# Optimization experiments

Measured on AMD Instinct MI355X. Metric: run time of the kernel, lower is better.

Reference implementation:

```python
import jax, jax.numpy as jnp
import numpy as np

EPS = 1e-5
LAMBDA_REG = 1.0
ALPHA_ENTROPY = 0.5
ALPHA_DIVERSITY = 0.5

B, N, D, K = 32, 1024, 256, 512  # batch, tokens, dim_embed, num_embed


def setup_inputs() -> dict:
    key = jax.random.key(0)
    k0, k1, k2 = jax.random.split(key, 3)
    inputs = jax.random.normal(k0, (B, N, D), dtype=jnp.float32)
    gamma = jnp.ones((D,), jnp.float32)
    beta = jnp.zeros((D,), jnp.float32)
    # keras 'uniform' initializer default: U(-0.05, 0.05)
    embed_w = jax.random.uniform(k1, (D, K), jnp.float32, -0.05, 0.05)
    # keras 'random_normal' default: stddev=0.05
    d_w = jax.random.normal(k2, (D, D), jnp.float32) * 0.05
    d_b = jnp.zeros((D,), jnp.float32)
    return {"inputs": inputs, "gamma": gamma, "beta": beta,
            "embed_w": embed_w, "d_w": d_w, "d_b": d_b}


def _project_columns_to_simplex(P_sol):
    # P_sol: (K, M); project each column onto the probability simplex.
    P_t = P_sol.T                                   # (M, K)
    sorted_P = -jnp.sort(-P_t, axis=1)              # descending
    cumsum = jnp.cumsum(sorted_P, axis=1)
    k = jnp.arange(1, K + 1, dtype=P_t.dtype)
    thresholds = (cumsum - 1.0) / k
    valid = (sorted_P > thresholds).astype(jnp.int32)
    max_idx = jnp.argmax(valid * jnp.arange(K, dtype=jnp.int32), axis=1)  # (M,)
    sel_cumsum = jnp.take_along_axis(cumsum, max_idx[:, None], axis=1)[:, 0]
    theta = (sel_cumsum - 1.0) / (max_idx.astype(P_t.dtype) + 1.0)
    return jax.nn.relu(P_t - theta[:, None]).T      # (K, M)


def _forward(inputs, gamma, beta, embed_w, d_w, d_b):
    # dense + layernorm
    x = jnp.matmul(inputs, d_w) + d_b
    mean = jnp.mean(x, axis=-1, keepdims=True)
    var = jnp.var(x, axis=-1, keepdims=True)
    x = gamma * ((x - mean) / jnp.sqrt(var + EPS)) + beta

    flat = x.reshape(-1, D)                          # (M, D)
    flat_sg = jax.lax.stop_gradient(flat)

    # hard assignment (VQ-style, on detached encodings)
    dists = (jnp.sum(flat_sg ** 2, axis=1, keepdims=True)
             + jnp.sum(embed_w ** 2, axis=0, keepdims=True)
             - 2.0 * jnp.matmul(flat_sg, embed_w))   # (M, K)
    assign = jnp.argmin(dists, axis=1)
    P_tilde = jax.nn.one_hot(assign, K, dtype=jnp.float32).T  # (K, M)

    # regularized least squares: (C^T C + lam I) P = C^T Z + lam P_tilde
    C = embed_w                                       # (D, K)
    Z = flat.T                                        # (D, M)
    A = jnp.matmul(C.T, C) + LAMBDA_REG * jnp.eye(K, dtype=jnp.float32)
    b = jnp.matmul(C.T, Z) + LAMBDA_REG * P_tilde     # (K, M)
    P_sol = jnp.linalg.solve(A, b)
    P_proj = _project_columns_to_simplex(P_sol)       # (K, M)

    out_P_proj = P_proj.T.reshape(B, N, K)

    # perplexity
    p_j = jnp.mean(out_P_proj, axis=(0, 1))
    p_j = jnp.clip(p_j, 1e-10, 1.0 - 1e-9)
    p_j = p_j / jnp.sum(p_j)
    entropy_bits = -jnp.sum(p_j * jnp.log(p_j) / jnp.log(2.0))
    perplexity = jnp.power(2.0, entropy_bits)

    Zq_flat = jnp.matmul(C, P_proj).T                 # (M, D)

    # entropy regularizer
    p_mean = jnp.mean(out_P_proj, axis=(0, 1))
    p_mn = p_mean / (jnp.sum(p_mean) + EPS)
    entropy_reg = -jnp.sum(p_mn * jnp.log(p_mn + EPS))

    # diversity loss on l2-normalized codebook columns
    norm_cb = embed_w / jnp.sqrt(jnp.maximum(jnp.sum(embed_w ** 2, axis=0, keepdims=True), 1e-12))
    sims = jnp.matmul(norm_cb.T, norm_cb)
    masked = sims * (1.0 - jnp.eye(K, dtype=jnp.float32))
    diversity_loss = jnp.mean(jax.nn.relu(masked))

    primary_loss = jnp.mean((Zq_flat - flat) ** 2)  # discrete_loss=False path
    loss = primary_loss + ALPHA_ENTROPY * entropy_reg + ALPHA_DIVERSITY * diversity_loss

    Zq = Zq_flat.reshape(B, N, D)
    return Zq, out_P_proj, loss, perplexity


def reference(inputs, gamma, beta, embed_w, d_w, d_b):
    return _forward(inputs, gamma, beta, embed_w, d_w, d_b)
```

## Files before the change

kernel.cpp:

```cpp
#include <hip/hip_runtime.h>
#include <math.h>


#define M_ 32768
#define D_ 256
#define K_ 512
#define TAU 0.006f

typedef short bf16x8 __attribute__((ext_vector_type(8)));
typedef unsigned short u16x8 __attribute__((ext_vector_type(8)));
typedef unsigned short u16x4 __attribute__((ext_vector_type(4)));
typedef float f32x4 __attribute__((ext_vector_type(4)));

#define LSTR 56

__device__ inline void split_rne(float f, unsigned short& h, unsigned short& l)
{
    unsigned int u = __float_as_uint(f);
    unsigned int uh = u + (0x7FFFu + ((u >> 16) & 1u));
    h = (unsigned short)(uh >> 16);
    float fh = __uint_as_float(((unsigned int)h) << 16);
    float r = f - fh;
    l = (unsigned short)(__float_as_uint(r) >> 16);
}

__device__ inline unsigned short rne16(float f)
{
    unsigned int u = __float_as_uint(f);
    u += 0x7FFFu + ((u >> 16) & 1u);
    return (unsigned short)(u >> 16);
}

template<int EPI>
__global__ __launch_bounds__(256)
void mfma_gemm(const unsigned short* __restrict__ Ah,
               const unsigned short* __restrict__ Bh,
               float* __restrict__ Out, int Kd, int N,
               const float* __restrict__ AinvM, const int* __restrict__ assign,
               const float* Zref, float* __restrict__ lossPart)
{
    __shared__ unsigned short sA[128*LSTR];
    __shared__ unsigned short sB[128*LSTR];
    __shared__ float red[256];
    const int tid = threadIdx.x;
    const int m0 = blockIdx.y * 128, n0 = blockIdx.x * 128;
    const int w = tid >> 6, lane = tid & 63;
    const int wr = (w & 1) * 64, wc = (w >> 1) * 64;
    const int cg = lane >> 4, cr = lane & 15;

    f32x4 acc[4][4];
    const f32x4 z4 = {0.f, 0.f, 0.f, 0.f};
#pragma unroll
    for (int i = 0; i < 4; ++i)
#pragma unroll
        for (int j = 0; j < 4; ++j) acc[i][j] = z4;

    const int sr = tid >> 1;
    const int sk = (tid & 1) * 16;
    const int soff = sr * LSTR + sk;
    const unsigned short* Agh = Ah + (size_t)(m0 + sr) * Kd + sk;
    const unsigned short* Bgh = Bh + (size_t)(n0 + sr) * Kd + sk;

    for (int kb = 0; kb < Kd; kb += 32) {
        *(u16x8*)&sA[soff]     = *(const u16x8*)(Agh + kb);
        *(u16x8*)&sA[soff + 8] = *(const u16x8*)(Agh + kb + 8);
        *(u16x8*)&sB[soff]     = *(const u16x8*)(Bgh + kb);
        *(u16x8*)&sB[soff + 8] = *(const u16x8*)(Bgh + kb + 8);
        __syncthreads();
        bf16x8 ah[4], bh[4];
#pragma unroll
        for (int f = 0; f < 4; ++f) {
            ah[f] = *(const bf16x8*)&sA[(wr + f*16 + cr) * LSTR + cg*8];
            bh[f] = *(const bf16x8*)&sB[(wc + f*16 + cr) * LSTR + cg*8];
        }
#pragma unroll
        for (int i = 0; i < 4; ++i)
#pragma unroll
            for (int j = 0; j < 4; ++j)
                acc[i][j] = __builtin_amdgcn_mfma_f32_16x16x32_bf16(ah[i], bh[j], acc[i][j], 0, 0, 0);
        __syncthreads();
    }

    if (EPI == 2) {
#pragma unroll
        for (int i = 0; i < 4; ++i) {
#pragma unroll
            for (int q = 0; q < 4; ++q) {
                const int row = m0 + wr + i*16 + cg*4 + q;
                const int am = assign[row];
                const float* Arow = AinvM + (size_t)am * K_ + n0 + wc;
#pragma unroll
                for (int j = 0; j < 4; ++j)
                    Out[(size_t)row * N + n0 + wc + j*16 + cr] =
                        acc[i][j][q] + Arow[j*16 + cr];
            }
        }
    } else {
        float lsum = 0.f;
#pragma unroll
        for (int i = 0; i < 4; ++i) {
#pragma unroll
            for (int q = 0; q < 4; ++q) {
                const int row = m0 + wr + i*16 + cg*4 + q;
#pragma unroll
                for (int j = 0; j < 4; ++j) {
                    const int col = n0 + wc + j*16 + cr;
                    const float v = acc[i][j][q];
                    const float zv = Zref[(size_t)row * N + col];
                    const float d = v - zv;
                    lsum += d * d;
                    Out[(size_t)row * N + col] = v;
                }
            }
        }
        red[tid] = lsum;
        __syncthreads();
        for (int s = 128; s > 0; s >>= 1) {
            if (tid < s) red[tid] += red[tid + s];
            __syncthreads();
        }
        if (tid == 0) lossPart[blockIdx.y * gridDim.x + blockIdx.x] = red[0];
    }
}

__global__ __launch_bounds__(256)
void score_mfma_argmin(const unsigned short* __restrict__ Zh, const unsigned short* __restrict__ Zl,
                       const unsigned short* __restrict__ Bth, const unsigned short* __restrict__ Btl,
                       const float* __restrict__ cn2, const float* __restrict__ zn2,
                       float* __restrict__ PV, float* __restrict__ PB,
                       int* __restrict__ PI)
{
    __shared__ unsigned short sAh[128*LSTR], sAl[128*LSTR];
    __shared__ unsigned short sBh[128*LSTR], sBl[128*LSTR];
    __shared__ float l1v[128][2], l2v[128][2];
    __shared__ int   liv[128][2];
    const int tid = threadIdx.x;
    const int m0 = blockIdx.y * 128, n0 = blockIdx.x * 128;
    const int w = tid >> 6, lane = tid & 63;
    const int wr = (w & 1) * 64, wc = (w >> 1) * 64;
    const int cg = lane >> 4, cr = lane & 15;

    f32x4 acc[4][4];
    const f32x4 z4 = {0.f, 0.f, 0.f, 0.f};
#pragma unroll
    for (int i = 0; i < 4; ++i)
#pragma unroll
        for (int j = 0; j < 4; ++j) acc[i][j] = z4;

    const int sr = tid >> 1;
    const int sk = (tid & 1) * 16;
    const int soff = sr * LSTR + sk;
    const unsigned short* Ah = Zh  + (size_t)(m0 + sr) * D_ + sk;
    const unsigned short* Al = Zl  + (size_t)(m0 + sr) * D_ + sk;
    const unsigned short* Bh = Bth + (size_t)(n0 + sr) * D_ + sk;
    const unsigned short* Bl = Btl + (size_t)(n0 + sr) * D_ + sk;

    for (int kb = 0; kb < D_; kb += 32) {
        *(u16x8*)&sAh[soff]     = *(const u16x8*)(Ah + kb);
        *(u16x8*)&sAh[soff + 8] = *(const u16x8*)(Ah + kb + 8);
        *(u16x8*)&sAl[soff]     = *(const u16x8*)(Al + kb);
        *(u16x8*)&sAl[soff + 8] = *(const u16x8*)(Al + kb + 8);
        *(u16x8*)&sBh[soff]     = *(const u16x8*)(Bh + kb);
        *(u16x8*)&sBh[soff + 8] = *(const u16x8*)(Bh + kb + 8);
        *(u16x8*)&sBl[soff]     = *(const u16x8*)(Bl + kb);
        *(u16x8*)&sBl[soff + 8] = *(const u16x8*)(Bl + kb + 8);
        __syncthreads();
        bf16x8 ah[4], al[4], bh[4], bl[4];
#pragma unroll
        for (int f = 0; f < 4; ++f) {
            const int ao = (wr + f*16 + cr) * LSTR + cg*8;
            ah[f] = *(const bf16x8*)&sAh[ao];
            al[f] = *(const bf16x8*)&sAl[ao];
            const int bo = (wc + f*16 + cr) * LSTR + cg*8;
            bh[f] = *(const bf16x8*)&sBh[bo];
            bl[f] = *(const bf16x8*)&sBl[bo];
        }
#pragma unroll
        for (int i = 0; i < 4; ++i)
#pragma unroll
            for (int j = 0; j < 4; ++j) {
                acc[i][j] = __builtin_amdgcn_mfma_f32_16x16x32_bf16(ah[i], bh[j], acc[i][j], 0, 0, 0);
                acc[i][j] = __builtin_amdgcn_mfma_f32_16x16x32_bf16(al[i], bh[j], acc[i][j], 0, 0, 0);
                acc[i][j] = __builtin_amdgcn_mfma_f32_16x16x32_bf16(ah[i], bl[j], acc[i][j], 0, 0, 0);
            }
        __syncthreads();
    }

    const int half = wc >> 6;
#pragma unroll
    for (int i = 0; i < 4; ++i) {
#pragma unroll
        for (int q = 0; q < 4; ++q) {
            const int rl = wr + i*16 + cg*4 + q;
            const float zr = zn2[m0 + rl];
            float b1 = 3.4e38f, b2 = 3.4e38f; int i1 = 0x7fffffff;
#pragma unroll
            for (int j = 0; j < 4; ++j) {
                const int col = n0 + wc + j*16 + cr;
                const float d = (zr + cn2[col]) - 2.0f * acc[i][j][q];
                if (d < b1 || (d == b1 && col < i1)) { b2 = b1; b1 = d; i1 = col; }
                else if (d < b2) b2 = d;
            }
#pragma unroll
            for (int off = 1; off < 16; off <<= 1) {
                const float o1 = __shfl_xor(b1, off);
                const int   oi = __shfl_xor(i1, off);
                const float o2 = __shfl_xor(b2, off);
                if (o1 < b1 || (o1 == b1 && oi < i1)) { b2 = fminf(b1, o2); b1 = o1; i1 = oi; }
                else { b2 = fminf(o1, b2); }
            }
            if (cr == 0) { l1v[rl][half] = b1; l2v[rl][half] = b2; liv[rl][half] = i1; }
        }
    }
    __syncthreads();
    if (tid < 128) {
        const float a1 = l1v[tid][0], a2 = l2v[tid][0]; const int ai = liv[tid][0];
        const float c1 = l1v[tid][1], c2 = l2v[tid][1]; const int ci = liv[tid][1];
        float b1, b2; int bi;
        if (c1 < a1 || (c1 == a1 && ci < ai)) { b1 = c1; bi = ci; b2 = fminf(a1, c2); }
        else { b1 = a1; bi = ai; b2 = fminf(c1, a2); }
        const size_t o = (size_t)(m0 + tid) * 4 + blockIdx.x;
        PV[o] = b1; PB[o] = b2; PI[o] = bi;
    }
}

__global__ void argmin_reduce4(const float* __restrict__ PV, const float* __restrict__ PB,
                               const int* __restrict__ PI, int* __restrict__ assign,
                               int* __restrict__ rlist, int* __restrict__ rcount)
{
    const int m = blockIdx.x * 256 + threadIdx.x;
    float b1 = PV[(size_t)m*4], b2 = PB[(size_t)m*4]; int i1 = PI[(size_t)m*4];
#pragma unroll
    for (int s = 1; s < 4; ++s) {
        const float o1 = PV[(size_t)m*4+s], o2 = PB[(size_t)m*4+s];
        const int oi = PI[(size_t)m*4+s];
        if (o1 < b1 || (o1 == b1 && oi < i1)) { b2 = fminf(b1, o2); b1 = o1; i1 = oi; }
        else { b2 = fminf(o1, b2); }
    }
    assign[m] = i1;
    if (b2 - b1 < TAU) { const int p = atomicAdd(rcount, 1); rlist[p] = m; }
}

__global__ __launch_bounds__(256)
void repair_gemm(const float* __restrict__ Z, const float* __restrict__ B,
                 const float* __restrict__ cn2, const float* __restrict__ zn2,
                 const int* __restrict__ rlist, const int* __restrict__ rcount,
                 float* __restrict__ PV, int* __restrict__ PI)
{
    const int n = rcount[0];
    const int m0 = blockIdx.y * 128;
    if (m0 >= n) return;
    __shared__ float As[16][132];
    __shared__ float Bs[16][128];
    __shared__ int rows_s[128];
    const int tid = threadIdx.x;
    const int tx = tid & 15, ty = tid >> 4;
    const int n0 = blockIdx.x * 128;

    if (tid < 128) rows_s[tid] = (m0 + tid < n) ? rlist[m0 + tid] : rlist[0];
    __syncthreads();

    float acc[8][8];
#pragma unroll
    for (int i = 0; i < 8; ++i)
#pragma unroll
        for (int j = 0; j < 8; ++j) acc[i][j] = 0.f;

    const int ar = tid >> 1, ac = (tid & 1) * 8;
    const int br = tid >> 4, bc = (tid & 15) * 8;
    const float* Ap = Z + (size_t)rows_s[ar] * D_ + ac;
    const float* Bp = B + (size_t)br * K_ + n0 + bc;

    for (int kb = 0; kb < D_; kb += 16) {
        float4 a0 = *(const float4*)(Ap + kb);
        float4 a1 = *(const float4*)(Ap + kb + 4);
        float4 b0 = *(const float4*)(Bp + (size_t)kb * K_);
        float4 b1 = *(const float4*)(Bp + (size_t)kb * K_ + 4);
        As[ac+0][ar] = a0.x; As[ac+1][ar] = a0.y; As[ac+2][ar] = a0.z; As[ac+3][ar] = a0.w;
        As[ac+4][ar] = a1.x; As[ac+5][ar] = a1.y; As[ac+6][ar] = a1.z; As[ac+7][ar] = a1.w;
        *(float4*)&Bs[br][bc]     = b0;
        *(float4*)&Bs[br][bc + 4] = b1;
        __syncthreads();
#pragma unroll
        for (int kk = 0; kk < 16; ++kk) {
            float4 av0 = *(const float4*)&As[kk][ty*4];
            float4 av1 = *(const float4*)&As[kk][64 + ty*4];
            float4 bv0 = *(const float4*)&Bs[kk][tx*4];
            float4 bv1 = *(const float4*)&Bs[kk][64 + tx*4];
            float a_[8] = {av0.x, av0.y, av0.z, av0.w, av1.x, av1.y, av1.z, av1.w};
            float b_[8] = {bv0.x, bv0.y, bv0.z, bv0.w, bv1.x, bv1.y, bv1.z, bv1.w};
#pragma unroll
            for (int i = 0; i < 8; ++i)
#pragma unroll
                for (int j = 0; j < 8; ++j)
                    acc[i][j] = fmaf(a_[i], b_[j], acc[i][j]);
        }
        __syncthreads();
    }

#pragma unroll
    for (int hi = 0; hi < 2; ++hi) {
#pragma unroll
        for (int i = 0; i < 4; ++i) {
            const int rl = hi*64 + ty*4 + i;
            if (m0 + rl >= n) continue;
            const float zr = zn2[rows_s[rl]];
            float best = 3.4e38f; int bi = 0x7fffffff;
#pragma unroll
            for (int hj = 0; hj < 2; ++hj) {
#pragma unroll
                for (int j = 0; j < 4; ++j) {
                    const int col = n0 + hj*64 + tx*4 + j;
                    const float t1 = zr + cn2[col];
                    const float d  = t1 - 2.0f * acc[hi*4+i][hj*4+j];
                    if (d < best) { best = d; bi = col; }
                }
            }
#pragma unroll
            for (int off = 1; off < 16; off <<= 1) {
                const float ov = __shfl_xor(best, off);
                const int   oi = __shfl_xor(bi, off);
                if (ov < best || (ov == best && oi < bi)) { best = ov; bi = oi; }
            }
            if (tx == 0) {
                PV[(size_t)(m0 + rl) * 4 + blockIdx.x] = best;
                PI[(size_t)(m0 + rl) * 4 + blockIdx.x] = bi;
            }
        }
    }
}

__global__ void repair_scatter(const float* __restrict__ PV, const int* __restrict__ PI,
                               const int* __restrict__ rlist, const int* __restrict__ rcount,
                               int* __restrict__ assign)
{
    const int r = blockIdx.x * 256 + threadIdx.x;
    if (r >= rcount[0]) return;
    float best = PV[(size_t)r * 4]; int bi = PI[(size_t)r * 4];
#pragma unroll
    for (int nb = 1; nb < 4; ++nb) {
        const float v = PV[(size_t)r * 4 + nb]; const int ix = PI[(size_t)r * 4 + nb];
        if (v < best || (v == best && ix < bi)) { best = v; bi = ix; }
    }
    assign[rlist[r]] = bi;
}

__global__ __launch_bounds__(256)
void dense_ln_kernel(const float* __restrict__ A, const float* __restrict__ Bw,
                     const float* __restrict__ bias, const float* __restrict__ gamma,
                     const float* __restrict__ beta, float* __restrict__ Z,
                     float* __restrict__ zn2,
                     unsigned short* __restrict__ Zh, unsigned short* __restrict__ Zl)
{
    __shared__ float As[16][68];
    __shared__ float Bs[16][260];
    __shared__ float rred[64][17];
    __shared__ float rstat[64];
    const int tid = threadIdx.x, tx = tid & 15, ty = tid >> 4;
    const int m0 = blockIdx.x * 64;
    float acc[4][16];
#pragma unroll
    for (int i = 0; i < 4; ++i)
#pragma unroll
        for (int j = 0; j < 16; ++j) acc[i][j] = 0.f;

    const int ar = tid >> 2, ac = (tid & 3) * 4;
    const int br = tid >> 4, bc = (tid & 15) * 16;
    for (int kb = 0; kb < 256; kb += 16) {
        float4 a = *(const float4*)(A + (size_t)(m0 + ar) * 256 + kb + ac);
        As[ac+0][ar] = a.x; As[ac+1][ar] = a.y; As[ac+2][ar] = a.z; As[ac+3][ar] = a.w;
#pragma unroll
        for (int q = 0; q < 4; ++q)
            *(float4*)&Bs[br][bc + q*4] =
                *(const float4*)(Bw + (size_t)(kb + br) * 256 + bc + q*4);
        __syncthreads();
#pragma unroll
        for (int kk = 0; kk < 16; ++kk) {
            float4 a4 = *(const float4*)&As[kk][ty*4];
            float av[4] = {a4.x, a4.y, a4.z, a4.w};
            float bv[16];
#pragma unroll
            for (int q = 0; q < 4; ++q) {
                float4 b4 = *(const float4*)&Bs[kk][q*64 + tx*4];
                bv[q*4+0] = b4.x; bv[q*4+1] = b4.y; bv[q*4+2] = b4.z; bv[q*4+3] = b4.w;
            }
#pragma unroll
            for (int i = 0; i < 4; ++i)
#pragma unroll
                for (int j = 0; j < 16; ++j)
                    acc[i][j] = fmaf(av[i], bv[j], acc[i][j]);
        }
        __syncthreads();
    }

    float bcol[16];
#pragma unroll
    for (int q = 0; q < 4; ++q) {
        float4 b4 = *(const float4*)(bias + q*64 + tx*4);
        bcol[q*4+0] = b4.x; bcol[q*4+1] = b4.y; bcol[q*4+2] = b4.z; bcol[q*4+3] = b4.w;
    }
#pragma unroll
    for (int i = 0; i < 4; ++i)
#pragma unroll
        for (int j = 0; j < 16; ++j) acc[i][j] += bcol[j];

#pragma unroll
    for (int i = 0; i < 4; ++i) {
        float s = 0.f;
#pragma unroll
        for (int j = 0; j < 16; ++j) s += acc[i][j];
        rred[ty*4+i][tx] = s;
    }
    __syncthreads();
    if (tid < 64) {
        float s = 0.f;
#pragma unroll
        for (int t = 0; t < 16; ++t) s += rred[tid][t];
        rstat[tid] = s * (1.f / 256.f);
    }
    __syncthreads();
    float mean_[4];
#pragma unroll
    for (int i = 0; i < 4; ++i) mean_[i] = rstat[ty*4+i];

#pragma unroll
    for (int i = 0; i < 4; ++i) {
        float s = 0.f;
#pragma unroll
        for (int j = 0; j < 16; ++j) { float d = acc[i][j] - mean_[i]; s += d * d; }
        rred[ty*4+i][tx] = s;
    }
    __syncthreads();
    if (tid < 64) {
        float s = 0.f;
#pragma unroll
        for (int t = 0; t < 16; ++t) s += rred[tid][t];
        rstat[tid] = s * (1.f / 256.f);
    }
    __syncthreads();
    float rstd_[4];
#pragma unroll
    for (int i = 0; i < 4; ++i) rstd_[i] = sqrtf(rstat[ty*4+i] + 1e-5f);

    float gam[16], bet[16];
#pragma unroll
    for (int q = 0; q < 4; ++q) {
        float4 g4 = *(const float4*)(gamma + q*64 + tx*4);
        float4 e4 = *(const float4*)(beta  + q*64 + tx*4);
        gam[q*4+0] = g4.x; gam[q*4+1] = g4.y; gam[q*4+2] = g4.z; gam[q*4+3] = g4.w;
        bet[q*4+0] = e4.x; bet[q*4+1] = e4.y; bet[q*4+2] = e4.z; bet[q*4+3] = e4.w;
    }
#pragma unroll
    for (int i = 0; i < 4; ++i)
#pragma unroll
        for (int j = 0; j < 16; ++j) {
            const float d = acc[i][j] - mean_[i];
            acc[i][j] = gam[j] * (d / rstd_[i]) + bet[j];
        }

#pragma unroll
    for (int i = 0; i < 4; ++i) {
        float s = 0.f;
#pragma unroll
        for (int j = 0; j < 16; ++j) s += acc[i][j] * acc[i][j];
        rred[ty*4+i][tx] = s;
    }
    __syncthreads();
    if (tid < 64) {
        float s = 0.f;
#pragma unroll
        for (int t = 0; t < 16; ++t) s += rred[tid][t];
        zn2[m0 + tid] = s;
    }

#pragma unroll
    for (int i = 0; i < 4; ++i) {
        const int row = m0 + ty*4 + i;
#pragma unroll
        for (int q = 0; q < 4; ++q) {
            float4 v;
            v.x = acc[i][q*4+0]; v.y = acc[i][q*4+1];
            v.z = acc[i][q*4+2]; v.w = acc[i][q*4+3];
            const size_t pos = (size_t)row * 256 + q*64 + tx*4;
            *(float4*)(Z + pos) = v;
            unsigned short h[4], l[4];
            split_rne(v.x, h[0], l[0]); split_rne(v.y, h[1], l[1]);
            split_rne(v.z, h[2], l[2]); split_rne(v.w, h[3], l[3]);
            *(u16x4*)(Zh + pos) = *(u16x4*)h;
            *(u16x4*)(Zl + pos) = *(u16x4*)l;
        }
    }
}

template<int TRA, int ASUM, int BSUM>
__global__ __launch_bounds__(256)
void sk_gemm(const float* __restrict__ A, const float* __restrict__ B,
             float* __restrict__ Out, int M, int N, int Kd)
{
    __shared__ float As[16][68];
    __shared__ float Bs[16][68];
    const int tid = threadIdx.x;
    const int tx = tid & 15, ty = tid >> 4;
    const int n0 = blockIdx.x * 64, m0 = blockIdx.y * 64;
    const int kw = Kd >> 2;
    const int kb0 = blockIdx.z * kw;
    const size_t aP = (size_t)M * Kd;
    const size_t bP = (size_t)Kd * N;
    float acc[4][4];
#pragma unroll
    for (int i = 0; i < 4; ++i)
#pragma unroll
        for (int j = 0; j < 4; ++j) acc[i][j] = 0.f;

    for (int kb = kb0; kb < kb0 + kw; kb += 16) {
        if (TRA == 0) {
            const int ar2 = tid >> 2, ac2 = (tid & 3) * 4;
            const size_t off = (size_t)(m0 + ar2) * Kd + kb + ac2;
            float4 a;
            if (ASUM) {
                float4 a0 = *(const float4*)(A + off);
                float4 a1 = *(const float4*)(A + aP + off);
                float4 a2 = *(const float4*)(A + 2*aP + off);
                float4 a3 = *(const float4*)(A + 3*aP + off);
                a.x = a0.x + a1.x + a2.x + a3.x;
                a.y = a0.y + a1.y + a2.y + a3.y;
                a.z = a0.z + a1.z + a2.z + a3.z;
                a.w = a0.w + a1.w + a2.w + a3.w;
                if (ASUM == 2) {
                    const int row = m0 + ar2, colb = kb + ac2;
                    if (row == colb)     a.x += 1.f;
                    if (row == colb + 1) a.y += 1.f;
                    if (row == colb + 2) a.z += 1.f;
                    if (row == colb + 3) a.w += 1.f;
                }
            } else {
                a = *(const float4*)(A + off);
            }
            As[ac2+0][ar2] = a.x; As[ac2+1][ar2] = a.y;
            As[ac2+2][ar2] = a.z; As[ac2+3][ar2] = a.w;
        } else {
            const int ar2 = tid >> 4, ac2 = (tid & 15) * 4;
            float4 a = *(const float4*)(A + (size_t)(kb + ar2) * M + m0 + ac2);
            *(float4*)&As[ar2][ac2] = a;
        }
        {
            const int br2 = tid >> 4, bc2 = (tid & 15) * 4;
            const size_t off = (size_t)(kb + br2) * N + n0 + bc2;
            float4 b;
            if (BSUM) {
                float4 b0 = *(const float4*)(B + off);
                float4 b1 = *(const float4*)(B + bP + off);
                float4 b2 = *(const float4*)(B + 2*bP + off);
                float4 b3 = *(const float4*)(B + 3*bP + off);
                b.x = b0.x + b1.x + b2.x + b3.x;
                b.y = b0.y + b1.y + b2.y + b3.y;
                b.z = b0.z + b1.z + b2.z + b3.z;
                b.w = b0.w + b1.w + b2.w + b3.w;
            } else {
                b = *(const float4*)(B + off);
            }
            *(float4*)&Bs[br2][bc2] = b;
        }
        __syncthreads();
#pragma unroll
        for (int kk = 0; kk < 16; ++kk) {
            float4 a4 = *(const float4*)&As[kk][ty*4];
            float4 b4 = *(const float4*)&Bs[kk][tx*4];
            float a_[4] = {a4.x, a4.y, a4.z, a4.w};
            float b_[4] = {b4.x, b4.y, b4.z, b4.w};
#pragma unroll
            for (int i = 0; i < 4; ++i)
#pragma unroll
                for (int j = 0; j < 4; ++j)
                    acc[i][j] = fmaf(a_[i], b_[j], acc[i][j]);
        }
        __syncthreads();
    }
    float* Op = Out + (size_t)blockIdx.z * M * N;
#pragma unroll
    for (int i = 0; i < 4; ++i)
#pragma unroll
        for (int j = 0; j < 4; ++j)
            Op[(size_t)(m0 + ty*4 + i) * N + n0 + tx*4 + j] = acc[i][j];
}

__global__ void xn_reduce(const float* __restrict__ Xc, const float* __restrict__ Xp,
                          float* __restrict__ Xn)
{
    const int idx = blockIdx.x * 256 + threadIdx.x;
    const float s = Xp[idx] + Xp[65536 + idx] + Xp[131072 + idx] + Xp[196608 + idx];
    Xn[idx] = 2.f * Xc[idx] - s;
}

__global__ void ainv_reduce(const float* __restrict__ Ap, float* __restrict__ Ainv)
{
    const int idx = blockIdx.x * 256 + threadIdx.x;
    const int i = idx >> 9, j = idx & 511;
    const float s = Ap[idx] + Ap[262144 + idx] + Ap[524288 + idx] + Ap[786432 + idx];
    Ainv[idx] = ((i == j) ? 1.f : 0.f) - s;
}

__global__ void g_reduce(const float* __restrict__ Gp, const float* __restrict__ cn2,
                         float* __restrict__ divPart)
{
    __shared__ float red[256];
    __shared__ float rsn[512];
    const int t = threadIdx.x;
    rsn[t]       = 1.f / sqrtf(fmaxf(cn2[t], 1e-12f));
    rsn[t + 256] = 1.f / sqrtf(fmaxf(cn2[t + 256], 1e-12f));
    __syncthreads();
    float dsum = 0.f;
#pragma unroll
    for (int e = 0; e < 4; ++e) {
        const int idx = blockIdx.x * 1024 + e * 256 + t;
        const int i = idx >> 9, j = idx & 511;
        const float g = Gp[idx] + Gp[262144 + idx] + Gp[524288 + idx] + Gp[786432 + idx];
        if (i != j) dsum += fmaxf(g * rsn[i] * rsn[j], 0.f);
    }
    red[t] = dsum; __syncthreads();
    for (int s = 128; s > 0; s >>= 1) {
        if (t < s) red[t] += red[t + s];
        __syncthreads();
    }
    if (t == 0) divPart[blockIdx.x] = red[0];
}

__global__ void rowabs_kernel(const float* __restrict__ Sp, float* __restrict__ rowAbs)
{
    __shared__ float red[256];
    const int r = blockIdx.x, t = threadIdx.x;
    const int idx = r * 256 + t;
    float v = Sp[idx] + Sp[65536 + idx] + Sp[131072 + idx] + Sp[196608 + idx];
    if (r == t) v += 1.f;
    red[t] = fabsf(v); __syncthreads();
    for (int s = 128; s > 0; s >>= 1) {
        if (t < s) red[t] += red[t + s];
        __syncthreads();
    }
    if (t == 0) rowAbs[r] = red[0];
}

__global__ void x1_init(const float* __restrict__ rowAbs, const float* __restrict__ Sp,
                        float* __restrict__ X)
{
    __shared__ float red[256];
    const int t = threadIdx.x;
    red[t] = rowAbs[t]; __syncthreads();
    for (int s = 128; s > 0; s >>= 1) {
        if (t < s) red[t] = fmaxf(red[t], red[t + s]);
        __syncthreads();
    }
    const float c = 2.f / (1.f + red[0]);
    const int idx = blockIdx.x * 256 + t;
    const int i = idx >> 8, j = idx & 255;
    float s4 = Sp[idx] + Sp[65536 + idx] + Sp[131072 + idx] + Sp[196608 + idx];
    if (i == j) s4 += 1.f;
    const float tt = c * s4;
    const float xp = c * tt;
    X[idx] = ((i == j) ? 2.f * c : 0.f) - xp;
}

__global__ void ut_reduce(const float* __restrict__ Up, unsigned short* __restrict__ Uth)
{
    const int idx = blockIdx.x * 256 + threadIdx.x;
    Uth[idx] = rne16(Up[idx] + Up[131072 + idx] + Up[262144 + idx] + Up[393216 + idx]);
}

__global__ void transpose_ct(const float* __restrict__ C, float* __restrict__ Ct,
                             unsigned short* __restrict__ Cth, unsigned short* __restrict__ Ctl)
{
    const int idx = blockIdx.x * 256 + threadIdx.x;
    const int k = idx >> 8, d = idx & 255;
    const float v = C[(size_t)d * K_ + k];
    Ct[idx] = v;
    unsigned short h, l;
    split_rne(v, h, l);
    Cth[idx] = h; Ctl[idx] = l;
}

__global__ void c_native(const float* __restrict__ C, unsigned short* __restrict__ Ch)
{
    const int idx = blockIdx.x * 256 + threadIdx.x;
    Ch[idx] = rne16(C[idx]);
}

__global__ void cn2_kernel(const float* __restrict__ C, float* __restrict__ cn2)
{
    const int k = blockIdx.x * 256 + threadIdx.x;
    float s = 0.f;
    for (int d = 0; d < D_; ++d) { float c = C[(size_t)d * K_ + k]; s = fmaf(c, c, s); }
    cn2[k] = s;
}

__global__ __launch_bounds__(1024)
void project_colsum_kernel(float* P, unsigned short* __restrict__ Ph,
                           float* __restrict__ part)
{
    __shared__ float ps[16][512];
    const int wave = threadIdx.x >> 6;
    const int lane = threadIdx.x & 63;
    float psum[8];
#pragma unroll
    for (int j = 0; j < 8; ++j) psum[j] = 0.f;

    for (int r = 0; r < 8; ++r) {
        const int row = blockIdx.x * 128 + wave * 8 + r;
        const size_t base = (size_t)row * K_ + lane;
        float v[8];
#pragma unroll
        for (int j = 0; j < 8; ++j) v[j] = P[base + j * 64];

        float s = 0.f;
#pragma unroll
        for (int j = 0; j < 8; ++j) s += v[j];
        for (int off = 32; off > 0; off >>= 1) s += __shfl_xor(s, off);

        float theta = (s - 1.f) * (1.f / 512.f);
        int cnt = K_;
        for (int it = 0; it < K_; ++it) {
            float ls = 0.f; int lc = 0;
#pragma unroll
            for (int j = 0; j < 8; ++j)
                if (v[j] > theta) { ls += v[j]; ++lc; }
            for (int off = 32; off > 0; off >>= 1) {
                ls += __shfl_xor(ls, off);
                lc += __shfl_xor(lc, off);
            }
            if (lc == cnt) break;
            theta = (ls - 1.f) / (float)lc;
            cnt = lc;
        }
#pragma unroll
        for (int j = 0; j < 8; ++j) {
            const float o = fmaxf(v[j] - theta, 0.f);
            P[base + j * 64] = o;
            Ph[base + j * 64] = rne16(o);
            psum[j] += o;
        }
    }
#pragma unroll
    for (int j = 0; j < 8; ++j) ps[wave][lane + j * 64] = psum[j];
    __syncthreads();
    for (int c = threadIdx.x; c < 512; c += 1024) {
        float s = 0.f;
#pragma unroll
        for (int wv = 0; wv < 16; ++wv) s += ps[wv][c];
        part[(size_t)blockIdx.x * K_ + c] = s;
    }
}

__global__ __launch_bounds__(512)
void part_reduce(const float* __restrict__ part, float* __restrict__ part2)
{
    const int t = threadIdx.x, b = blockIdx.x;
    float s = 0.f;
    for (int r = 0; r < 16; ++r) s += part[(size_t)(b * 16 + r) * K_ + t];
    part2[(size_t)b * K_ + t] = s;
}

#define BLOCK_REDUCE_512(val, result) \
    red[t] = (val); __syncthreads(); \
    for (int s_ = 256; s_ > 0; s_ >>= 1) { if (t < s_) red[t] += red[t + s_]; __syncthreads(); } \
    result = red[0]; __syncthreads();

__global__ __launch_bounds__(512)
void finalize_kernel(const float* __restrict__ part2, const float* __restrict__ divPart,
                     const float* __restrict__ lossPart, float* __restrict__ out_scal)
{
    __shared__ float red[512];
    const int t = threadIdx.x;

    float praw = 0.f;
    for (int b = 0; b < 16; ++b) praw += part2[b * K_ + t];
    const float pm = praw * (1.f / 32768.f);

    const float pj = fminf(fmaxf(pm, 1e-10f), 1.0f);
    float sp; BLOCK_REDUCE_512(pj, sp);
    const float pjn = pj / sp;
    float Hbits; BLOCK_REDUCE_512(-pjn * logf(pjn) / 0.69314718056f, Hbits);

    float spm; BLOCK_REDUCE_512(pm, spm);
    const float s2 = spm + 1e-5f;
    const float pmn = pm / s2;
    float ereg; BLOCK_REDUCE_512(-pmn * logf(pmn + 1e-5f), ereg);

    float dv = (t < 256) ? divPart[t] : 0.f;
    float divs; BLOCK_REDUCE_512(dv, divs);
    const float divloss = divs * (1.f / 262144.f);

    float lp = lossPart[t];
    float prim; BLOCK_REDUCE_512(lp, prim);
    prim *= 1.f / 8388608.f;

    if (t == 0) {
        out_scal[0] = prim + 0.5f * ereg + 0.5f * divloss;
        out_scal[1] = exp2f(Hbits);
    }
}

extern "C" void kernel_launch(void* const* d_in, const int* in_sizes, int n_in,
                              void* d_out, int out_size, void* d_ws, size_t ws_size,
                              hipStream_t stream)
{
    const float* inputs = (const float*)d_in[0];
    const float* gamma  = (const float*)d_in[1];
    const float* beta   = (const float*)d_in[2];
    const float* C      = (const float*)d_in[3];
    const float* d_w    = (const float*)d_in[4];
    const float* d_b    = (const float*)d_in[5];

    float* out = (float*)d_out;
    float* Z = out;
    float* P = out + (size_t)M_ * D_;
    float* out_scal = P + (size_t)M_ * K_;

    float* w = (float*)d_ws;
    float* Sp   = w;     w += 4 * 65536;
    float* Tp   = w;     w += 4 * 65536;
    float* Xp   = w;     w += 4 * 65536;
    float* Up   = w;     w += 4 * 131072;
    float* Ap   = w;     w += 4 * 262144;
    float* Xa   = w;     w += 65536;
    float* Xb   = w;     w += 65536;
    float* Ainv = w;     w += 262144;
    float* Ct   = w;     w += 131072;
    float* cn2  = w;     w += 512;
    float* rowAbs = w;   w += 256;
    float* zn2  = w;     w += M_;
    float* part = w;     w += 256 * K_;
    float* part2 = w;    w += 16 * K_;
    float* lossPart = w; w += 512;
    float* divPart  = w; w += 256;
    float* PV   = w;     w += M_ * 4;
    float* PB   = w;     w += M_ * 4;
    int* PI     = (int*)w; w += M_ * 4;
    int* rlist  = (int*)w; w += M_;
    int* rcount = (int*)w; w += 16;
    int* assign = (int*)w; w += M_;
    unsigned short* Zh  = (unsigned short*)w; w += M_ * D_ / 2;
    unsigned short* Zl  = (unsigned short*)w; w += M_ * D_ / 2;
    unsigned short* Cth = (unsigned short*)w; w += (K_ * D_) / 2;
    unsigned short* Ctl = (unsigned short*)w; w += (K_ * D_) / 2;
    unsigned short* Ch  = (unsigned short*)w; w += (K_ * D_) / 2;
    unsigned short* Uth = (unsigned short*)w; w += (K_ * D_) / 2;
    unsigned short* Ph  = Zh;

    hipMemsetAsync(rcount, 0, sizeof(int), stream);

    dense_ln_kernel<<<M_/64, 256, 0, stream>>>(inputs, d_w, d_b, gamma, beta, Z, zn2, Zh, Zl);
    transpose_ct<<<(K_ * D_) / 256, 256, 0, stream>>>(C, Ct, Cth, Ctl);
    c_native<<<(K_ * D_) / 256, 256, 0, stream>>>(C, Ch);
    cn2_kernel<<<K_ / 256, 256, 0, stream>>>(C, cn2);
    sk_gemm<1, 0, 0><<<dim3(4, 4, 4), 256, 0, stream>>>(Ct, Ct, Sp, 256, 256, 512);
    rowabs_kernel<<<256, 256, 0, stream>>>(Sp, rowAbs);
    x1_init<<<256, 256, 0, stream>>>(rowAbs, Sp, Xa);
    float* Xc = Xa; float* Xn = Xb;
    for (int it = 0; it < 3; ++it) {
        sk_gemm<0, 2, 0><<<dim3(4, 4, 4), 256, 0, stream>>>(Sp, Xc, Tp, 256, 256, 256);
        sk_gemm<0, 0, 1><<<dim3(4, 4, 4), 256, 0, stream>>>(Xc, Tp, Xp, 256, 256, 256);
        xn_reduce<<<256, 256, 0, stream>>>(Xc, Xp, Xn);
        float* tmp = Xc; Xc = Xn; Xn = tmp;
    }
    sk_gemm<1, 0, 0><<<dim3(4, 8, 4), 256, 0, stream>>>(C, Xc, Up, 512, 256, 256);
    sk_gemm<0, 1, 0><<<dim3(8, 8, 4), 256, 0, stream>>>(Up, C, Ap, 512, 512, 256);
    ainv_reduce<<<1024, 256, 0, stream>>>(Ap, Ainv);
    sk_gemm<1, 0, 0><<<dim3(8, 8, 4), 256, 0, stream>>>(C, C, Ap, 512, 512, 256);
    g_reduce<<<256, 256, 0, stream>>>(Ap, cn2, divPart);
    ut_reduce<<<512, 256, 0, stream>>>(Up, Uth);
    score_mfma_argmin<<<dim3(K_/128, M_/128), 256, 0, stream>>>(Zh, Zl, Cth, Ctl, cn2, zn2, PV, PB, PI);
    argmin_reduce4<<<M_/256, 256, 0, stream>>>(PV, PB, PI, assign, rlist, rcount);
    repair_gemm<<<dim3(K_/128, M_/128), 256, 0, stream>>>(Z, C, cn2, zn2, rlist, rcount, PV, PI);
    repair_scatter<<<M_/256, 256, 0, stream>>>(PV, PI, rlist, rcount, assign);
    mfma_gemm<2><<<dim3(K_/128, M_/128), 256, 0, stream>>>(
        Zh, Uth, P, D_, K_, Ainv, assign, nullptr, nullptr);
    project_colsum_kernel<<<M_/128, 1024, 0, stream>>>(P, Ph, part);
    part_reduce<<<16, 512, 0, stream>>>(part, part2);
    mfma_gemm<3><<<dim3(D_/128, M_/128), 256, 0, stream>>>(
        Ph, Ch, Z, K_, D_, nullptr, nullptr, Z, lossPart);
    finalize_kernel<<<1, 512, 0, stream>>>(part2, divPart, lossPart, out_scal);

    (void)in_sizes; (void)n_in; (void)out_size; (void)ws_size;
}
```

Before: 394.2 us.

## Fuse small reductions into GEMM epilogues, merge C prep kernels, double-buffer dense LN

Several small follow-up kernels are folded into neighbouring ones. The split-K reductions for X and Ainv move into GEMM epilogues, and the C transpose, cast and norm kernels merge into one prep_c kernel that also zeroes rcount in place of the memset. The Ut and G reductions are combined, and repair_gemm now loops over all K columns inside one block so the scatter kernel goes away. dense_ln gets double-buffered shared-memory staging. This cuts launch overhead and intermediate traffic, at the cost of mfma_gemm<2> re-reading four Ap partials per output element, which adds global loads.

```diff
diff --git a/kernel.cpp b/kernel.cpp
--- a/kernel.cpp
+++ b/kernel.cpp
@@ -36,7 +36,7 @@
 void mfma_gemm(const unsigned short* __restrict__ Ah,
                const unsigned short* __restrict__ Bh,
                float* __restrict__ Out, int Kd, int N,
-               const float* __restrict__ AinvM, const int* __restrict__ assign,
+               const float* __restrict__ Ap, const int* __restrict__ assign,
                const float* Zref, float* __restrict__ lossPart)
 {
     __shared__ unsigned short sA[128*LSTR];
@@ -88,11 +88,14 @@
             for (int q = 0; q < 4; ++q) {
                 const int row = m0 + wr + i*16 + cg*4 + q;
                 const int am = assign[row];
-                const float* Arow = AinvM + (size_t)am * K_ + n0 + wc;
-#pragma unroll
-                for (int j = 0; j < 4; ++j)
-                    Out[(size_t)row * N + n0 + wc + j*16 + cr] =
-                        acc[i][j][q] + Arow[j*16 + cr];
+#pragma unroll
+                for (int j = 0; j < 4; ++j) {
+                    const int col = n0 + wc + j*16 + cr;
+                    const size_t o = (size_t)am * K_ + col;
+                    const float s = Ap[o] + Ap[262144 + o] + Ap[524288 + o] + Ap[786432 + o];
+                    const float g = ((am == col) ? 1.f : 0.f) - s;
+                    Out[(size_t)row * N + col] = acc[i][j][q] + g;
+                }
             }
         }
     } else {
@@ -245,104 +248,99 @@
 void repair_gemm(const float* __restrict__ Z, const float* __restrict__ B,
                  const float* __restrict__ cn2, const float* __restrict__ zn2,
                  const int* __restrict__ rlist, const int* __restrict__ rcount,
-                 float* __restrict__ PV, int* __restrict__ PI)
+                 int* __restrict__ assign)
 {
     const int n = rcount[0];
-    const int m0 = blockIdx.y * 128;
+    const int m0 = blockIdx.x * 128;
     if (m0 >= n) return;
     __shared__ float As[16][132];
     __shared__ float Bs[16][128];
     __shared__ int rows_s[128];
+    __shared__ float rbv[128];
+    __shared__ int   rbi[128];
     const int tid = threadIdx.x;
     const int tx = tid & 15, ty = tid >> 4;
-    const int n0 = blockIdx.x * 128;
-
-    if (tid < 128) rows_s[tid] = (m0 + tid < n) ? rlist[m0 + tid] : rlist[0];
-    __syncthreads();
-
-    float acc[8][8];
-#pragma unroll
-    for (int i = 0; i < 8; ++i)
-#pragma unroll
-        for (int j = 0; j < 8; ++j) acc[i][j] = 0.f;
+
+    if (tid < 128) {
+        rows_s[tid] = (m0 + tid < n) ? rlist[m0 + tid] : rlist[0];
+        rbv[tid] = 3.4e38f; rbi[tid] = 0x7fffffff;
+    }
+    __syncthreads();
 
     const int ar = tid >> 1, ac = (tid & 1) * 8;
     const int br = tid >> 4, bc = (tid & 15) * 8;
-    const float* Ap = Z + (size_t)rows_s[ar] * D_ + ac;
-    const float* Bp = B + (size_t)br * K_ + n0 + bc;
-
-    for (int kb = 0; kb < D_; kb += 16) {
-        float4 a0 = *(const float4*)(Ap + kb);
-        float4 a1 = *(const float4*)(Ap + kb + 4);
-        float4 b0 = *(const float4*)(Bp + (size_t)kb * K_);
-        float4 b1 = *(const float4*)(Bp + (size_t)kb * K_ + 4);
-        As[ac+0][ar] = a0.x; As[ac+1][ar] = a0.y; As[ac+2][ar] = a0.z; As[ac+3][ar] = a0.w;
-        As[ac+4][ar] = a1.x; As[ac+5][ar] = a1.y; As[ac+6][ar] = a1.z; As[ac+7][ar] = a1.w;
-        *(float4*)&Bs[br][bc]     = b0;
-        *(float4*)&Bs[br][bc + 4] = b1;
-        __syncthreads();
-#pragma unroll
-        for (int kk = 0; kk < 16; ++kk) {
-            float4 av0 = *(const float4*)&As[kk][ty*4];
-            float4 av1 = *(const float4*)&As[kk][64 + ty*4];
-            float4 bv0 = *(const float4*)&Bs[kk][tx*4];
-            float4 bv1 = *(const float4*)&Bs[kk][64 + tx*4];
-            float a_[8] = {av0.x, av0.y, av0.z, av0.w, av1.x, av1.y, av1.z, av1.w};
-            float b_[8] = {bv0.x, bv0.y, bv0.z, bv0.w, bv1.x, bv1.y, bv1.z, bv1.w};
-#pragma unroll
-            for (int i = 0; i < 8; ++i)
-#pragma unroll
-                for (int j = 0; j < 8; ++j)
-                    acc[i][j] = fmaf(a_[i], b_[j], acc[i][j]);
-        }
-        __syncthreads();
-    }
-
-#pragma unroll
-    for (int hi = 0; hi < 2; ++hi) {
-#pragma unroll
-        for (int i = 0; i < 4; ++i) {
-            const int rl = hi*64 + ty*4 + i;
-            if (m0 + rl >= n) continue;
-            const float zr = zn2[rows_s[rl]];
-            float best = 3.4e38f; int bi = 0x7fffffff;
-#pragma unroll
-            for (int hj = 0; hj < 2; ++hj) {
-#pragma unroll
-                for (int j = 0; j < 4; ++j) {
-                    const int col = n0 + hj*64 + tx*4 + j;
-                    const float t1 = zr + cn2[col];
-                    const float d  = t1 - 2.0f * acc[hi*4+i][hj*4+j];
-                    if (d < best) { best = d; bi = col; }
+    const float* Apt = Z + (size_t)rows_s[ar] * D_ + ac;
+
+    for (int ns = 0; ns < 4; ++ns) {
+        const int n0 = ns * 128;
+        float acc[8][8];
+#pragma unroll
+        for (int i = 0; i < 8; ++i)
+#pragma unroll
+            for (int j = 0; j < 8; ++j) acc[i][j] = 0.f;
+        const float* Bp = B + (size_t)br * K_ + n0 + bc;
+
+        for (int kb = 0; kb < D_; kb += 16) {
+            float4 a0 = *(const float4*)(Apt + kb);
+            float4 a1 = *(const float4*)(Apt + kb + 4);
+            float4 b0 = *(const float4*)(Bp + (size_t)kb * K_);
+            float4 b1 = *(const float4*)(Bp + (size_t)kb * K_ + 4);
+            As[ac+0][ar] = a0.x; As[ac+1][ar] = a0.y; As[ac+2][ar] = a0.z; As[ac+3][ar] = a0.w;
+            As[ac+4][ar] = a1.x; As[ac+5][ar] = a1.y; As[ac+6][ar] = a1.z; As[ac+7][ar] = a1.w;
+            *(float4*)&Bs[br][bc]     = b0;
+            *(float4*)&Bs[br][bc + 4] = b1;
+            __syncthreads();
+#pragma unroll
+            for (int kk = 0; kk < 16; ++kk) {
+                float4 av0 = *(const float4*)&As[kk][ty*4];
+                float4 av1 = *(const float4*)&As[kk][64 + ty*4];
+                float4 bv0 = *(const float4*)&Bs[kk][tx*4];
+                float4 bv1 = *(const float4*)&Bs[kk][64 + tx*4];
+                float a_[8] = {av0.x, av0.y, av0.z, av0.w, av1.x, av1.y, av1.z, av1.w};
+                float b_[8] = {bv0.x, bv0.y, bv0.z, bv0.w, bv1.x, bv1.y, bv1.z, bv1.w};
+#pragma unroll
+                for (int i = 0; i < 8; ++i)
+#pragma unroll
+                    for (int j = 0; j < 8; ++j)
+                        acc[i][j] = fmaf(a_[i], b_[j], acc[i][j]);
+            }
+            __syncthreads();
+        }
+
+#pragma unroll
+        for (int hi = 0; hi < 2; ++hi) {
+#pragma unroll
+            for (int i = 0; i < 4; ++i) {
+                const int rl = hi*64 + ty*4 + i;
+                if (m0 + rl >= n) continue;
+                const float zr = zn2[rows_s[rl]];
+                float best = 3.4e38f; int bi = 0x7fffffff;
+#pragma unroll
+                for (int hj = 0; hj < 2; ++hj) {
+#pragma unroll
+                    for (int j = 0; j < 4; ++j) {
+                        const int col = n0 + hj*64 + tx*4 + j;
+                        const float t1 = zr + cn2[col];
+                        const float d  = t1 - 2.0f * acc[hi*4+i][hj*4+j];
+                        if (d < best) { best = d; bi = col; }
+                    }
                 }
-            }
-#pragma unroll
-            for (int off = 1; off < 16; off <<= 1) {
-                const float ov = __shfl_xor(best, off);
-                const int   oi = __shfl_xor(bi, off);
-                if (ov < best || (ov == best && oi < bi)) { best = ov; bi = oi; }
-            }
-            if (tx == 0) {
-                PV[(size_t)(m0 + rl) * 4 + blockIdx.x] = best;
-                PI[(size_t)(m0 + rl) * 4 + blockIdx.x] = bi;
-            }
-        }
-    }
-}
-
-__global__ void repair_scatter(const float* __restrict__ PV, const int* __restrict__ PI,
-                               const int* __restrict__ rlist, const int* __restrict__ rcount,
-                               int* __restrict__ assign)
-{
-    const int r = blockIdx.x * 256 + threadIdx.x;
-    if (r >= rcount[0]) return;
-    float best = PV[(size_t)r * 4]; int bi = PI[(size_t)r * 4];
-#pragma unroll
-    for (int nb = 1; nb < 4; ++nb) {
-        const float v = PV[(size_t)r * 4 + nb]; const int ix = PI[(size_t)r * 4 + nb];
-        if (v < best || (v == best && ix < bi)) { best = v; bi = ix; }
-    }
-    assign[rlist[r]] = bi;
+#pragma unroll
+                for (int off = 1; off < 16; off <<= 1) {
+                    const float ov = __shfl_xor(best, off);
+                    const int   oi = __shfl_xor(bi, off);
+                    if (ov < best || (ov == best && oi < bi)) { best = ov; bi = oi; }
+                }
+                if (tx == 0) {
+                    if (best < rbv[rl] || (best == rbv[rl] && bi < rbi[rl])) {
+                        rbv[rl] = best; rbi[rl] = bi;
+                    }
+                }
+            }
+        }
+        __syncthreads();
+    }
+    if (tid < 128 && m0 + tid < n) assign[rows_s[tid]] = rbi[tid];
 }
 
 __global__ __launch_bounds__(256)
@@ -352,8 +350,8 @@
                      float* __restrict__ zn2,
                      unsigned short* __restrict__ Zh, unsigned short* __restrict__ Zl)
 {
-    __shared__ float As[16][68];
-    __shared__ float Bs[16][260];
+    __shared__ float As[2][16][68];
+    __shared__ float Bs[2][16][260];
     __shared__ float rred[64][17];
     __shared__ float rstat[64];
     const int tid = threadIdx.x, tx = tid & 15, ty = tid >> 4;
@@ -366,22 +364,29 @@
 
     const int ar = tid >> 2, ac = (tid & 3) * 4;
     const int br = tid >> 4, bc = (tid & 15) * 16;
-    for (int kb = 0; kb < 256; kb += 16) {
-        float4 a = *(const float4*)(A + (size_t)(m0 + ar) * 256 + kb + ac);
-        As[ac+0][ar] = a.x; As[ac+1][ar] = a.y; As[ac+2][ar] = a.z; As[ac+3][ar] = a.w;
-#pragma unroll
-        for (int q = 0; q < 4; ++q)
-            *(float4*)&Bs[br][bc + q*4] =
-                *(const float4*)(Bw + (size_t)(kb + br) * 256 + bc + q*4);
-        __syncthreads();
+
+#define DL_STAGE(buf, kb) { \
+    float4 a = *(const float4*)(A + (size_t)(m0 + ar) * 256 + (kb) + ac); \
+    As[buf][ac+0][ar] = a.x; As[buf][ac+1][ar] = a.y; \
+    As[buf][ac+2][ar] = a.z; As[buf][ac+3][ar] = a.w; \
+    _Pragma("unroll") \
+    for (int q = 0; q < 4; ++q) \
+        *(float4*)&Bs[buf][br][bc + q*4] = \
+            *(const float4*)(Bw + (size_t)((kb) + br) * 256 + bc + q*4); }
+
+    DL_STAGE(0, 0)
+    __syncthreads();
+    for (int t16 = 0; t16 < 16; ++t16) {
+        const int cur = t16 & 1;
+        if (t16 < 15) DL_STAGE(cur ^ 1, (t16 + 1) * 16)
 #pragma unroll
         for (int kk = 0; kk < 16; ++kk) {
-            float4 a4 = *(const float4*)&As[kk][ty*4];
+            float4 a4 = *(const float4*)&As[cur][kk][ty*4];
             float av[4] = {a4.x, a4.y, a4.z, a4.w};
             float bv[16];
 #pragma unroll
             for (int q = 0; q < 4; ++q) {
-                float4 b4 = *(const float4*)&Bs[kk][q*64 + tx*4];
+                float4 b4 = *(const float4*)&Bs[cur][kk][q*64 + tx*4];
                 bv[q*4+0] = b4.x; bv[q*4+1] = b4.y; bv[q*4+2] = b4.z; bv[q*4+3] = b4.w;
             }
 #pragma unroll
@@ -392,6 +397,7 @@
         }
         __syncthreads();
     }
+#undef DL_STAGE
 
     float bcol[16];
 #pragma unroll
@@ -492,10 +498,11 @@
     }
 }
 
-template<int TRA, int ASUM, int BSUM>
+template<int TRA, int ASUM, int BSUM, int OEPI>
 __global__ __launch_bounds__(256)
 void sk_gemm(const float* __restrict__ A, const float* __restrict__ B,
-             float* __restrict__ Out, int M, int N, int Kd)
+             float* __restrict__ Out, int M, int N, int Kd,
+             const float* __restrict__ Xprev)
 {
     __shared__ float As[16][68];
     __shared__ float Bs[16][68];
@@ -576,53 +583,47 @@
         }
         __syncthreads();
     }
-    float* Op = Out + (size_t)blockIdx.z * M * N;
+    const size_t MN = (size_t)M * N;
+    float* Op = Out + (size_t)blockIdx.z * MN;
 #pragma unroll
     for (int i = 0; i < 4; ++i)
 #pragma unroll
-        for (int j = 0; j < 4; ++j)
-            Op[(size_t)(m0 + ty*4 + i) * N + n0 + tx*4 + j] = acc[i][j];
-}
-
-__global__ void xn_reduce(const float* __restrict__ Xc, const float* __restrict__ Xp,
-                          float* __restrict__ Xn)
-{
-    const int idx = blockIdx.x * 256 + threadIdx.x;
-    const float s = Xp[idx] + Xp[65536 + idx] + Xp[131072 + idx] + Xp[196608 + idx];
-    Xn[idx] = 2.f * Xc[idx] - s;
-}
-
-__global__ void ainv_reduce(const float* __restrict__ Ap, float* __restrict__ Ainv)
-{
-    const int idx = blockIdx.x * 256 + threadIdx.x;
-    const int i = idx >> 9, j = idx & 511;
-    const float s = Ap[idx] + Ap[262144 + idx] + Ap[524288 + idx] + Ap[786432 + idx];
-    Ainv[idx] = ((i == j) ? 1.f : 0.f) - s;
-}
-
-__global__ void g_reduce(const float* __restrict__ Gp, const float* __restrict__ cn2,
-                         float* __restrict__ divPart)
+        for (int j = 0; j < 4; ++j) {
+            const size_t idx = (size_t)(m0 + ty*4 + i) * N + n0 + tx*4 + j;
+            if (OEPI == 0) {
+                Op[idx] = acc[i][j];
+            } else {
+                float base = 0.f;
+                if (blockIdx.z == 0)
+                    base = 2.f * (Xprev[idx] + Xprev[MN + idx] +
+                                  Xprev[2*MN + idx] + Xprev[3*MN + idx]);
+                Op[idx] = base - acc[i][j];
+            }
+        }
+}
+
+__global__ __launch_bounds__(256)
+void prep_c(const float* __restrict__ C, float* __restrict__ Ct,
+            unsigned short* __restrict__ Cth, unsigned short* __restrict__ Ctl,
+            unsigned short* __restrict__ Ch, float* __restrict__ cn2,
+            int* __restrict__ rcount)
 {
     __shared__ float red[256];
-    __shared__ float rsn[512];
-    const int t = threadIdx.x;
-    rsn[t]       = 1.f / sqrtf(fmaxf(cn2[t], 1e-12f));
-    rsn[t + 256] = 1.f / sqrtf(fmaxf(cn2[t + 256], 1e-12f));
-    __syncthreads();
-    float dsum = 0.f;
-#pragma unroll
-    for (int e = 0; e < 4; ++e) {
-        const int idx = blockIdx.x * 1024 + e * 256 + t;
-        const int i = idx >> 9, j = idx & 511;
-        const float g = Gp[idx] + Gp[262144 + idx] + Gp[524288 + idx] + Gp[786432 + idx];
-        if (i != j) dsum += fmaxf(g * rsn[i] * rsn[j], 0.f);
-    }
-    red[t] = dsum; __syncthreads();
-    for (int s = 128; s > 0; s >>= 1) {
-        if (t < s) red[t] += red[t + s];
-        __syncthreads();
-    }
-    if (t == 0) divPart[blockIdx.x] = red[0];
+    const int k = blockIdx.x, t = threadIdx.x;
+    const float v = C[(size_t)t * K_ + k];
+    Ct[k * 256 + t] = v;
+    unsigned short h, l;
+    split_rne(v, h, l);
+    Cth[k * 256 + t] = h;
+    Ctl[k * 256 + t] = l;
+    Ch[(size_t)t * K_ + k] = h;
+    red[t] = v * v;
+    __syncthreads();
+    for (int s = 128; s > 0; s >>= 1) { if (t < s) red[t] += red[t + s]; __syncthreads(); }
+    if (t == 0) {
+        cn2[k] = red[0];
+        if (k == 0) rcount[0] = 0;
+    }
 }
 
 __global__ void rowabs_kernel(const float* __restrict__ Sp, float* __restrict__ rowAbs)
@@ -641,7 +642,7 @@
 }
 
 __global__ void x1_init(const float* __restrict__ rowAbs, const float* __restrict__ Sp,
-                        float* __restrict__ X)
+                        float* __restrict__ Xp)
 {
     __shared__ float red[256];
     const int t = threadIdx.x;
@@ -657,39 +658,43 @@
     if (i == j) s4 += 1.f;
     const float tt = c * s4;
     const float xp = c * tt;
-    X[idx] = ((i == j) ? 2.f * c : 0.f) - xp;
-}
-
-__global__ void ut_reduce(const float* __restrict__ Up, unsigned short* __restrict__ Uth)
-{
-    const int idx = blockIdx.x * 256 + threadIdx.x;
-    Uth[idx] = rne16(Up[idx] + Up[131072 + idx] + Up[262144 + idx] + Up[393216 + idx]);
-}
-
-__global__ void transpose_ct(const float* __restrict__ C, float* __restrict__ Ct,
-                             unsigned short* __restrict__ Cth, unsigned short* __restrict__ Ctl)
-{
-    const int idx = blockIdx.x * 256 + threadIdx.x;
-    const int k = idx >> 8, d = idx & 255;
-    const float v = C[(size_t)d * K_ + k];
-    Ct[idx] = v;
-    unsigned short h, l;
-    split_rne(v, h, l);
-    Cth[idx] = h; Ctl[idx] = l;
-}
-
-__global__ void c_native(const float* __restrict__ C, unsigned short* __restrict__ Ch)
-{
-    const int idx = blockIdx.x * 256 + threadIdx.x;
-    Ch[idx] = rne16(C[idx]);
-}
-
-__global__ void cn2_kernel(const float* __restrict__ C, float* __restrict__ cn2)
-{
-    const int k = blockIdx.x * 256 + threadIdx.x;
-    float s = 0.f;
-    for (int d = 0; d < D_; ++d) { float c = C[(size_t)d * K_ + k]; s = fmaf(c, c, s); }
-    cn2[k] = s;
+    Xp[idx] = ((i == j) ? 2.f * c : 0.f) - xp;
+    Xp[65536 + idx]  = 0.f;
+    Xp[131072 + idx] = 0.f;
+    Xp[196608 + idx] = 0.f;
+}
+
+__global__ __launch_bounds__(256)
+void gut_reduce(const float* __restrict__ Up, unsigned short* __restrict__ Uth,
+                const float* __restrict__ Gp, const float* __restrict__ cn2,
+                float* __restrict__ divPart)
+{
+    __shared__ float red[256];
+    __shared__ float rsn[512];
+    const int b = blockIdx.x, t = threadIdx.x;
+    if (b < 512) {
+        const int idx = b * 256 + t;
+        Uth[idx] = rne16(Up[idx] + Up[131072 + idx] + Up[262144 + idx] + Up[393216 + idx]);
+        return;
+    }
+    const int gb = b - 512;
+    rsn[t]       = 1.f / sqrtf(fmaxf(cn2[t], 1e-12f));
+    rsn[t + 256] = 1.f / sqrtf(fmaxf(cn2[t + 256], 1e-12f));
+    __syncthreads();
+    float dsum = 0.f;
+#pragma unroll
+    for (int e = 0; e < 4; ++e) {
+        const int idx = gb * 1024 + e * 256 + t;
+        const int i = idx >> 9, j = idx & 511;
+        const float g = Gp[idx] + Gp[262144 + idx] + Gp[524288 + idx] + Gp[786432 + idx];
+        if (i != j) dsum += fmaxf(g * rsn[i] * rsn[j], 0.f);
+    }
+    red[t] = dsum; __syncthreads();
+    for (int s = 128; s > 0; s >>= 1) {
+        if (t < s) red[t] += red[t + s];
+        __syncthreads();
+    }
+    if (t == 0) divPart[gb] = red[0];
 }
 
 __global__ __launch_bounds__(1024)
@@ -817,12 +822,11 @@
     float* w = (float*)d_ws;
     float* Sp   = w;     w += 4 * 65536;
     float* Tp   = w;     w += 4 * 65536;
-    float* Xp   = w;     w += 4 * 65536;
+    float* XpA  = w;     w += 4 * 65536;
+    float* XpB  = w;     w += 4 * 65536;
     float* Up   = w;     w += 4 * 131072;
     float* Ap   = w;     w += 4 * 262144;
-    float* Xa   = w;     w += 65536;
-    float* Xb   = w;     w += 65536;
-    float* Ainv = w;     w += 262144;
+    float* Gp   = w;     w += 4 * 262144;
     float* Ct   = w;     w += 131072;
     float* cn2  = w;     w += 512;
     float* rowAbs = w;   w += 256;
@@ -845,34 +849,26 @@
     unsigned short* Uth = (unsigned short*)w; w += (K_ * D_) / 2;
     unsigned short* Ph  = Zh;
 
-    hipMemsetAsync(rcount, 0, sizeof(int), stream);
-
     dense_ln_kernel<<<M_/64, 256, 0, stream>>>(inputs, d_w, d_b, gamma, beta, Z, zn2, Zh, Zl);
-    transpose_ct<<<(K_ * D_) / 256, 256, 0, stream>>>(C, Ct, Cth, Ctl);
-    c_native<<<(K_ * D_) / 256, 256, 0, stream>>>(C, Ch);
-    cn2_kernel<<<K_ / 256, 256, 0, stream>>>(C, cn2);
-    sk_gemm<1, 0, 0><<<dim3(4, 4, 4), 256, 0, stream>>>(Ct, Ct, Sp, 256, 256, 512);
+    prep_c<<<K_, 256, 0, stream>>>(C, Ct, Cth, Ctl, Ch, cn2, rcount);
+    sk_gemm<1, 0, 0, 0><<<dim3(4, 4, 4), 256, 0, stream>>>(Ct, Ct, Sp, 256, 256, 512, nullptr);
     rowabs_kernel<<<256, 256, 0, stream>>>(Sp, rowAbs);
-    x1_init<<<256, 256, 0, stream>>>(rowAbs, Sp, Xa);
-    float* Xc = Xa; float* Xn = Xb;
+    x1_init<<<256, 256, 0, stream>>>(rowAbs, Sp, XpA);
+    float* Xc = XpA; float* Xn = XpB;
     for (int it = 0; it < 3; ++it) {
-        sk_gemm<0, 2, 0><<<dim3(4, 4, 4), 256, 0, stream>>>(Sp, Xc, Tp, 256, 256, 256);
-        sk_gemm<0, 0, 1><<<dim3(4, 4, 4), 256, 0, stream>>>(Xc, Tp, Xp, 256, 256, 256);
-        xn_reduce<<<256, 256, 0, stream>>>(Xc, Xp, Xn);
+        sk_gemm<0, 2, 1, 0><<<dim3(4, 4, 4), 256, 0, stream>>>(Sp, Xc, Tp, 256, 256, 256, nullptr);
+        sk_gemm<0, 1, 1, 1><<<dim3(4, 4, 4), 256, 0, stream>>>(Xc, Tp, Xn, 256, 256, 256, Xc);
         float* tmp = Xc; Xc = Xn; Xn = tmp;
     }
-    sk_gemm<1, 0, 0><<<dim3(4, 8, 4), 256, 0, stream>>>(C, Xc, Up, 512, 256, 256);
-    sk_gemm<0, 1, 0><<<dim3(8, 8, 4), 256, 0, stream>>>(Up, C, Ap, 512, 512, 256);
-    ainv_reduce<<<1024, 256, 0, stream>>>(Ap, Ainv);
-    sk_gemm<1, 0, 0><<<dim3(8, 8, 4), 256, 0, stream>>>(C, C, Ap, 512, 512, 256);
-    g_reduce<<<256, 256, 0, stream>>>(Ap, cn2, divPart);
-    ut_reduce<<<512, 256, 0, stream>>>(Up, Uth);
+    sk_gemm<1, 0, 1, 0><<<dim3(4, 8, 4), 256, 0, stream>>>(C, Xc, Up, 512, 256, 256, nullptr);
+    sk_gemm<0, 1, 0, 0><<<dim3(8, 8, 4), 256, 0, stream>>>(Up, C, Ap, 512, 512, 256, nullptr);
+    sk_gemm<1, 0, 0, 0><<<dim3(8, 8, 4), 256, 0, stream>>>(C, C, Gp, 512, 512, 256, nullptr);
+    gut_reduce<<<768, 256, 0, stream>>>(Up, Uth, Gp, cn2, divPart);
     score_mfma_argmin<<<dim3(K_/128, M_/128), 256, 0, stream>>>(Zh, Zl, Cth, Ctl, cn2, zn2, PV, PB, PI);
     argmin_reduce4<<<M_/256, 256, 0, stream>>>(PV, PB, PI, assign, rlist, rcount);
-    repair_gemm<<<dim3(K_/128, M_/128), 256, 0, stream>>>(Z, C, cn2, zn2, rlist, rcount, PV, PI);
-    repair_scatter<<<M_/256, 256, 0, stream>>>(PV, PI, rlist, rcount, assign);
+    repair_gemm<<<M_/128, 256, 0, stream>>>(Z, C, cn2, zn2, rlist, rcount, assign);
     mfma_gemm<2><<<dim3(K_/128, M_/128), 256, 0, stream>>>(
-        Zh, Uth, P, D_, K_, Ainv, assign, nullptr, nullptr);
+        Zh, Uth, P, D_, K_, Ap, assign, nullptr, nullptr);
     project_colsum_kernel<<<M_/128, 1024, 0, stream>>>(P, Ph, part);
     part_reduce<<<16, 512, 0, stream>>>(part, part2);
     mfma_gemm<3><<<dim3(D_/128, M_/128), 256, 0, stream>>>(
```

Measured after the change: 498.6 us. 26.5% more time.
